# Performance work log

Measured on AMD Instinct MI355X. Metric: run time of the kernel, lower is better.

Reference implementation:

```python
import jax, jax.numpy as jnp
import numpy as np

N_NODES = 50000
N_EDGES = 800000
NFEAT = 256
NHID = 128
LATENT = 64


def setup_inputs() -> dict:
    key = jax.random.key(0)
    ks = jax.random.split(key, 8)
    x = jax.random.normal(ks[0], (N_NODES, NFEAT), dtype=jnp.float32)
    src = jax.random.randint(ks[1], (N_EDGES,), 0, N_NODES, dtype=jnp.int32)
    dst = jax.random.randint(ks[2], (N_EDGES,), 0, N_NODES, dtype=jnp.int32)
    edge_weight = jax.random.uniform(ks[3], (N_EDGES,), dtype=jnp.float32)
    W1 = jax.random.normal(ks[4], (NFEAT, NHID), dtype=jnp.float32) / np.sqrt(NFEAT)
    b1 = jnp.zeros((NHID,), dtype=jnp.float32)
    Wmu = jax.random.normal(ks[5], (NHID, LATENT), dtype=jnp.float32) / np.sqrt(NHID)
    bmu = jnp.zeros((LATENT,), dtype=jnp.float32)
    Wlv = jax.random.normal(ks[6], (NHID, LATENT), dtype=jnp.float32) / np.sqrt(NHID)
    blv = jnp.zeros((LATENT,), dtype=jnp.float32)
    return {"x": x, "src": src, "dst": dst, "edge_weight": edge_weight,
            "W1": W1, "b1": b1, "Wmu": Wmu, "bmu": bmu, "Wlv": Wlv, "blv": blv}


def gcn_conv(x, W, b, src, dst, edge_weight, n_nodes):
    # GCNConv: linear transform then sparse (weighted) adjacency aggregation.
    h = x @ W                                   # [N, out]
    msg = h[src] * edge_weight[:, None]         # [E, out] gather + scale
    agg = jax.ops.segment_sum(msg, dst, num_segments=n_nodes)  # scatter-add
    return agg + b


def reference(x, src, dst, edge_weight, W1, b1, Wmu, bmu, Wlv, blv):
    h = jax.nn.relu(gcn_conv(x, W1, b1, src, dst, edge_weight, N_NODES))
    mu = gcn_conv(h, Wmu, bmu, src, dst, edge_weight, N_NODES)
    logvar = gcn_conv(h, Wlv, blv, src, dst, edge_weight, N_NODES)
    return (mu, logvar)
```

## Files before the change

### kernel.cpp

```cpp
#include <hip/hip_runtime.h>
#include <hip/hip_bf16.h>

#define N_NODES 50000
#define N_EDGES 800000
#define NFEAT 256
#define NHID 128
#define LATENT 64
#define NB 98
#define BSH 9
#define CT 4096
#define CBLK 196

typedef __attribute__((ext_vector_type(8))) short bf16x8;
typedef __attribute__((ext_vector_type(4))) float f32x4;
typedef __attribute__((ext_vector_type(4))) short short4v;
typedef __attribute__((ext_vector_type(8))) short short8v;
typedef __attribute__((ext_vector_type(8))) unsigned short ushort8v;

__device__ inline unsigned short f2bf(float f) {
  union { float f; unsigned u; } c; c.f = f;
  unsigned r = (c.u + 0x7FFFu + ((c.u >> 16) & 1u)) >> 16;
  return (unsigned short)r;
}
__device__ inline float bf2f(unsigned short u) {
  union { unsigned u; float f; } c; c.u = ((unsigned)u) << 16;
  return c.f;
}

__launch_bounds__(256)
__global__ void prep_w_kernel(const float* __restrict__ W1,
                              const float* __restrict__ Wmu,
                              const float* __restrict__ Wlv,
                              unsigned short* __restrict__ W1T,
                              unsigned short* __restrict__ WcT) {
  int b = blockIdx.x;
  int t = threadIdx.x;
  if (b < 128) {
    W1T[b * NFEAT + t] = f2bf(W1[(size_t)t * NHID + b]);
  } else {
    int n = b - 128;
    if (t < NHID) {
      float v = (n < 64) ? Wmu[(size_t)t * LATENT + n]
                         : Wlv[(size_t)t * LATENT + (n - 64)];
      WcT[n * NHID + t] = f2bf(v);
    }
  }
}

__launch_bounds__(256)
__global__ void gemm1_kernel(const float* __restrict__ X,
                             const unsigned short* __restrict__ W1T,
                             unsigned short* __restrict__ XWb) {
  __shared__ short A_lds[64][40];
  const int t = threadIdx.x;
  const int lane = t & 63;
  const int wave = t >> 6;
  const int row0 = blockIdx.x * 64;
  const int l15 = lane & 15, quad = lane >> 4;
  const int srow = t >> 2, skg = t & 3;

  f32x4 acc[4][2];
#pragma unroll
  for (int i = 0; i < 4; i++)
#pragma unroll
    for (int j = 0; j < 2; j++) acc[i][j] = (f32x4){0.f, 0.f, 0.f, 0.f};

  for (int k0 = 0; k0 < NFEAT; k0 += 32) {
    int gr = row0 + srow;
    float4 v0, v1;
    if (gr < N_NODES) {
      const float* p = X + (size_t)gr * NFEAT + k0 + skg * 8;
      v0 = *(const float4*)p;
      v1 = *(const float4*)(p + 4);
    } else {
      v0 = make_float4(0.f, 0.f, 0.f, 0.f);
      v1 = v0;
    }
    short8v s;
    s[0] = f2bf(v0.x); s[1] = f2bf(v0.y); s[2] = f2bf(v0.z); s[3] = f2bf(v0.w);
    s[4] = f2bf(v1.x); s[5] = f2bf(v1.y); s[6] = f2bf(v1.z); s[7] = f2bf(v1.w);
    __syncthreads();
    *(short8v*)&A_lds[srow][skg * 8] = s;
    __syncthreads();

    bf16x8 a[4], b[2];
#pragma unroll
    for (int mt = 0; mt < 4; mt++)
      a[mt] = *(const bf16x8*)&A_lds[mt * 16 + l15][quad * 8];
#pragma unroll
    for (int nt = 0; nt < 2; nt++) {
      int n = wave * 32 + nt * 16 + l15;
      b[nt] = *(const bf16x8*)(W1T + (size_t)n * NFEAT + k0 + quad * 8);
    }
#pragma unroll
    for (int mt = 0; mt < 4; mt++)
#pragma unroll
      for (int nt = 0; nt < 2; nt++)
        acc[mt][nt] = __builtin_amdgcn_mfma_f32_16x16x32_bf16(a[mt], b[nt], acc[mt][nt], 0, 0, 0);
  }
#pragma unroll
  for (int mt = 0; mt < 4; mt++) {
#pragma unroll
    for (int reg = 0; reg < 4; reg++) {
      int gr = row0 + mt * 16 + quad * 4 + reg;
      if (gr < N_NODES) {
#pragma unroll
        for (int nt = 0; nt < 2; nt++) {
          int gc = wave * 32 + nt * 16 + l15;
          XWb[(size_t)gr * NHID + gc] = f2bf(acc[mt][nt][reg]);
        }
      }
    }
  }
}

__launch_bounds__(256)
__global__ void gemm2_kernel(const unsigned short* __restrict__ AGGb,
                             const float* __restrict__ b1,
                             const unsigned short* __restrict__ WcT,
                             unsigned short* __restrict__ Tb) {
  __shared__ short A_lds[64][40];
  const int t = threadIdx.x;
  const int lane = t & 63;
  const int wave = t >> 6;
  const int row0 = blockIdx.x * 64;
  const int l15 = lane & 15, quad = lane >> 4;
  const int srow = t >> 2, skg = t & 3;

  f32x4 acc[4][2];
#pragma unroll
  for (int i = 0; i < 4; i++)
#pragma unroll
    for (int j = 0; j < 2; j++) acc[i][j] = (f32x4){0.f, 0.f, 0.f, 0.f};

  for (int k0 = 0; k0 < NHID; k0 += 32) {
    int gr = row0 + srow;
    const float* bp = b1 + k0 + skg * 8;
    float4 bb0 = *(const float4*)bp;
    float4 bb1 = *(const float4*)(bp + 4);
    float bb[8] = {bb0.x, bb0.y, bb0.z, bb0.w, bb1.x, bb1.y, bb1.z, bb1.w};
    ushort8v raw;
    if (gr < N_NODES) {
      raw = *(const ushort8v*)(AGGb + (size_t)gr * NHID + k0 + skg * 8);
    } else {
#pragma unroll
      for (int k = 0; k < 8; k++) raw[k] = 0;
    }
    short8v s;
#pragma unroll
    for (int k = 0; k < 8; k++)
      s[k] = f2bf(fmaxf(bf2f(raw[k]) + bb[k], 0.f));
    __syncthreads();
    *(short8v*)&A_lds[srow][skg * 8] = s;
    __syncthreads();

    bf16x8 a[4], b[2];
#pragma unroll
    for (int mt = 0; mt < 4; mt++)
      a[mt] = *(const bf16x8*)&A_lds[mt * 16 + l15][quad * 8];
#pragma unroll
    for (int nt = 0; nt < 2; nt++) {
      int n = wave * 32 + nt * 16 + l15;
      b[nt] = *(const bf16x8*)(WcT + (size_t)n * NHID + k0 + quad * 8);
    }
#pragma unroll
    for (int mt = 0; mt < 4; mt++)
#pragma unroll
      for (int nt = 0; nt < 2; nt++)
        acc[mt][nt] = __builtin_amdgcn_mfma_f32_16x16x32_bf16(a[mt], b[nt], acc[mt][nt], 0, 0, 0);
  }
#pragma unroll
  for (int mt = 0; mt < 4; mt++) {
#pragma unroll
    for (int reg = 0; reg < 4; reg++) {
      int gr = row0 + mt * 16 + quad * 4 + reg;
      if (gr < N_NODES) {
#pragma unroll
        for (int nt = 0; nt < 2; nt++) {
          int gc = wave * 32 + nt * 16 + l15;
          Tb[(size_t)gr * NHID + gc] = f2bf(acc[mt][nt][reg]);
        }
      }
    }
  }
}

__launch_bounds__(256)
__global__ void coarse_hist_kernel(const int* __restrict__ dst,
                                   int* __restrict__ chist) {
  __shared__ int h[NB];
  int t = threadIdx.x;
  if (t < NB) h[t] = 0;
  __syncthreads();
  int base = blockIdx.x * CT;
#pragma unroll
  for (int k = 0; k < 16; k++) {
    int e = base + t + k * 256;
    if (e < N_EDGES) atomicAdd(&h[dst[e] >> BSH], 1);
  }
  __syncthreads();
  if (t < NB && h[t]) atomicAdd(&chist[t], h[t]);
}

__launch_bounds__(128)
__global__ void coarse_scan_kernel(const int* __restrict__ chist,
                                   int* __restrict__ coff,
                                   int* __restrict__ bcur) {
  __shared__ int lds[128];
  int t = threadIdx.x;
  int v = (t < NB) ? chist[t] : 0;
  lds[t] = v;
  __syncthreads();
  int x = v;
  for (int ofs = 1; ofs < 128; ofs <<= 1) {
    int y = (t >= ofs) ? lds[t - ofs] : 0;
    __syncthreads();
    x += y;
    lds[t] = x;
    __syncthreads();
  }
  if (t < NB) {
    int o = x - v;
    coff[t] = o;
    bcur[t] = o;
  }
  if (t == NB) coff[NB] = N_EDGES;
}

__launch_bounds__(256)
__global__ void coarse_part_kernel(const int* __restrict__ src,
                                   const int* __restrict__ dst,
                                   const float* __restrict__ ew,
                                   int* __restrict__ bcur,
                                   int2* __restrict__ part) {
  __shared__ int hist[NB], start[NB], cur[NB], gbase[NB];
  __shared__ int sc[128];
  __shared__ int2 stage[CT];
  int t = threadIdx.x;
  if (t < NB) hist[t] = 0;
  __syncthreads();
  int base = blockIdx.x * CT;
#pragma unroll
  for (int k = 0; k < 16; k++) {
    int e = base + t + k * 256;
    if (e < N_EDGES) atomicAdd(&hist[dst[e] >> BSH], 1);
  }
  __syncthreads();
  int v = (t < NB) ? hist[t] : 0;
  if (t < 128) sc[t] = v;
  __syncthreads();
  int x = v;
  for (int ofs = 1; ofs < 128; ofs <<= 1) {
    int y = (t >= ofs && t < 128) ? sc[t - ofs] : 0;
    __syncthreads();
    if (t < 128) { x += y; sc[t] = x; }
    __syncthreads();
  }
  if (t < NB) {
    int st = x - v;
    start[t] = st;
    cur[t] = st;
    gbase[t] = atomicAdd(&bcur[t], hist[t]);
  }
  __syncthreads();
#pragma unroll
  for (int k = 0; k < 16; k++) {
    int e = base + t + k * 256;
    if (e < N_EDGES) {
      int d = dst[e];
      int b = d >> BSH;
      int lp = atomicAdd(&cur[b], 1);
      stage[lp] = make_int2((src[e] << 16) | d, __float_as_int(ew[e]));
    }
  }
  __syncthreads();
  int nedge = min(CT, N_EDGES - base);
  for (int i = t; i < nedge; i += 256) {
    int2 e = stage[i];
    int b = (e.x & 0xffff) >> BSH;
    part[gbase[b] + (i - start[b])] = e;
  }
}

__launch_bounds__(256)
__global__ void fine_kernel(const int* __restrict__ coff,
                            const int2* __restrict__ part,
                            int* __restrict__ off,
                            int2* __restrict__ edata) {
  __shared__ int nh[512];
  __shared__ int sc[256];
  int t = threadIdx.x;
  int b = blockIdx.x;
  int beg = coff[b], end = coff[b + 1];
  int nb = b << BSH;
  nh[t] = 0;
  nh[t + 256] = 0;
  __syncthreads();
  for (int i = beg + t; i < end; i += 256) {
    int d = part[i].x & 0xffff;
    atomicAdd(&nh[d - nb], 1);
  }
  __syncthreads();
  int a0 = nh[2 * t], a1 = nh[2 * t + 1];
  int s = a0 + a1;
  sc[t] = s;
  __syncthreads();
  int x = s;
  for (int ofs = 1; ofs < 256; ofs <<= 1) {
    int y = (t >= ofs) ? sc[t - ofs] : 0;
    __syncthreads();
    x += y;
    sc[t] = x;
    __syncthreads();
  }
  int pairExcl = x - s;
  int e0 = beg + pairExcl;
  int e1 = beg + pairExcl + a0;
  __syncthreads();
  nh[2 * t] = e0;
  nh[2 * t + 1] = e1;
  int g0 = nb + 2 * t, g1 = nb + 2 * t + 1;
  if (g0 <= N_NODES) off[g0] = e0;
  if (g1 <= N_NODES) off[g1] = e1;
  __syncthreads();
  for (int i = beg + t; i < end; i += 256) {
    int2 e = part[i];
    int d = e.x & 0xffff;
    int pos = atomicAdd(&nh[d - nb], 1);
    edata[pos] = make_int2((int)(((unsigned)e.x) >> 16), e.y);
  }
}

__launch_bounds__(256)
__global__ void gather1_kernel(const unsigned short* __restrict__ XWb,
                               const int* __restrict__ off,
                               const int2* __restrict__ edata,
                               unsigned short* __restrict__ aggb) {
  int gw = (int)((blockIdx.x * blockDim.x + threadIdx.x) >> 6);
  if (gw >= N_NODES) return;
  int lane = threadIdx.x & 63;
  int q = lane >> 4;
  int c8 = lane & 15;
  int beg = off[gw], end = off[gw + 1];
  float acc[8];
#pragma unroll
  for (int k = 0; k < 8; k++) acc[k] = 0.f;
  int j = beg + q;
  for (; j + 4 < end; j += 8) {
    int2 e0 = edata[j];
    int2 e1 = edata[j + 4];
    ushort8v r0 = *(const ushort8v*)(XWb + (size_t)e0.x * NHID + c8 * 8);
    ushort8v r1 = *(const ushort8v*)(XWb + (size_t)e1.x * NHID + c8 * 8);
    float w0 = __int_as_float(e0.y);
    float w1 = __int_as_float(e1.y);
#pragma unroll
    for (int k = 0; k < 8; k++) acc[k] += bf2f(r0[k]) * w0;
#pragma unroll
    for (int k = 0; k < 8; k++) acc[k] += bf2f(r1[k]) * w1;
  }
  if (j < end) {
    int2 e0 = edata[j];
    ushort8v r0 = *(const ushort8v*)(XWb + (size_t)e0.x * NHID + c8 * 8);
    float w0 = __int_as_float(e0.y);
#pragma unroll
    for (int k = 0; k < 8; k++) acc[k] += bf2f(r0[k]) * w0;
  }
#pragma unroll
  for (int k = 0; k < 8; k++) {
    acc[k] += __shfl_down(acc[k], 32, 64);
    acc[k] += __shfl_down(acc[k], 16, 64);
  }
  if (lane < 16) {
    ushort8v st;
#pragma unroll
    for (int k = 0; k < 8; k++) st[k] = f2bf(acc[k]);
    *(ushort8v*)(aggb + (size_t)gw * NHID + c8 * 8) = st;
  }
}

__launch_bounds__(256)
__global__ void gather2_kernel(const unsigned short* __restrict__ Tb,
                               const int* __restrict__ off,
                               const int2* __restrict__ edata,
                               const float* __restrict__ bmu,
                               const float* __restrict__ blv,
                               float* __restrict__ out) {
  int gw = (int)((blockIdx.x * blockDim.x + threadIdx.x) >> 6);
  if (gw >= N_NODES) return;
  int lane = threadIdx.x & 63;
  int q = lane >> 4;
  int c8 = lane & 15;
  int beg = off[gw], end = off[gw + 1];
  float acc[8];
#pragma unroll
  for (int k = 0; k < 8; k++) acc[k] = 0.f;
  int j = beg + q;
  for (; j + 4 < end; j += 8) {
    int2 e0 = edata[j];
    int2 e1 = edata[j + 4];
    ushort8v r0 = *(const ushort8v*)(Tb + (size_t)e0.x * NHID + c8 * 8);
    ushort8v r1 = *(const ushort8v*)(Tb + (size_t)e1.x * NHID + c8 * 8);
    float w0 = __int_as_float(e0.y);
    float w1 = __int_as_float(e1.y);
#pragma unroll
    for (int k = 0; k < 8; k++) acc[k] += bf2f(r0[k]) * w0;
#pragma unroll
    for (int k = 0; k < 8; k++) acc[k] += bf2f(r1[k]) * w1;
  }
  if (j < end) {
    int2 e0 = edata[j];
    ushort8v r0 = *(const ushort8v*)(Tb + (size_t)e0.x * NHID + c8 * 8);
    float w0 = __int_as_float(e0.y);
#pragma unroll
    for (int k = 0; k < 8; k++) acc[k] += bf2f(r0[k]) * w0;
  }
#pragma unroll
  for (int k = 0; k < 8; k++) {
    acc[k] += __shfl_down(acc[k], 32, 64);
    acc[k] += __shfl_down(acc[k], 16, 64);
  }
  if (lane < 8) {
    const float* bp = bmu + c8 * 8;
    float4 b0 = *(const float4*)bp;
    float4 b1v = *(const float4*)(bp + 4);
    float* op = out + (size_t)gw * LATENT + c8 * 8;
    float4 o0, o1;
    o0.x = acc[0] + b0.x; o0.y = acc[1] + b0.y;
    o0.z = acc[2] + b0.z; o0.w = acc[3] + b0.w;
    o1.x = acc[4] + b1v.x; o1.y = acc[5] + b1v.y;
    o1.z = acc[6] + b1v.z; o1.w = acc[7] + b1v.w;
    *(float4*)op = o0;
    *(float4*)(op + 4) = o1;
  } else if (lane < 16) {
    int c = c8 - 8;
    const float* bp = blv + c * 8;
    float4 b0 = *(const float4*)bp;
    float4 b1v = *(const float4*)(bp + 4);
    float* op = out + (size_t)N_NODES * LATENT + (size_t)gw * LATENT + c * 8;
    float4 o0, o1;
    o0.x = acc[0] + b0.x; o0.y = acc[1] + b0.y;
    o0.z = acc[2] + b0.z; o0.w = acc[3] + b0.w;
    o1.x = acc[4] + b1v.x; o1.y = acc[5] + b1v.y;
    o1.z = acc[6] + b1v.z; o1.w = acc[7] + b1v.w;
    *(float4*)op = o0;
    *(float4*)(op + 4) = o1;
  }
}

extern "C" void kernel_launch(void* const* d_in, const int* in_sizes, int n_in,
                              void* d_out, int out_size, void* d_ws, size_t ws_size,
                              hipStream_t stream) {
  const float* x   = (const float*)d_in[0];
  const int*   src = (const int*)d_in[1];
  const int*   dst = (const int*)d_in[2];
  const float* ew  = (const float*)d_in[3];
  const float* W1  = (const float*)d_in[4];
  const float* b1  = (const float*)d_in[5];
  const float* Wmu = (const float*)d_in[6];
  const float* bmu = (const float*)d_in[7];
  const float* Wlv = (const float*)d_in[8];
  const float* blv = (const float*)d_in[9];
  float* out = (float*)d_out;

  unsigned short* bufb = (unsigned short*)d_ws;
  unsigned short* aggb = bufb + (size_t)N_NODES * NHID;
  int2* part  = (int2*)(aggb + (size_t)N_NODES * NHID);
  int2* edata = part + N_EDGES;
  int* off    = (int*)(edata + N_EDGES);
  int* chist  = off + 50048;
  int* coff   = chist + 128;
  int* bcur   = coff + 128;
  unsigned short* W1T = (unsigned short*)(bcur + 128);
  unsigned short* WcT = W1T + 128 * NFEAT;

  dim3 blk(256);
  int gemm_grid = (N_NODES + 63) / 64;
  int wave_grid = (N_NODES * 64 + 255) / 256;

  hipMemsetAsync(chist, 0, 128 * sizeof(int), stream);

  prep_w_kernel<<<256, blk, 0, stream>>>(W1, Wmu, Wlv, W1T, WcT);
  gemm1_kernel<<<gemm_grid, blk, 0, stream>>>(x, W1T, bufb);
  coarse_hist_kernel<<<CBLK, blk, 0, stream>>>(dst, chist);
  coarse_scan_kernel<<<1, 128, 0, stream>>>(chist, coff, bcur);
  coarse_part_kernel<<<CBLK, blk, 0, stream>>>(src, dst, ew, bcur, part);
  fine_kernel<<<NB, blk, 0, stream>>>(coff, part, off, edata);

  gather1_kernel<<<wave_grid, blk, 0, stream>>>(bufb, off, edata, aggb);
  gemm2_kernel<<<gemm_grid, blk, 0, stream>>>(aggb, b1, WcT, bufb);
  gather2_kernel<<<wave_grid, blk, 0, stream>>>(bufb, off, edata, bmu, blv, out);
}
```

Baseline: 253.1 us.

## Fuse first aggregation into second GEMM and drop global histogram/scan passes

Removes the coarse histogram and scan kernels by giving each coarse bucket a fixed-capacity slot region (CAP) in the partition buffer, with bucket counters zeroed inside the weight-prep kernel. The fine pass now uses 512 threads and emits (begin,end) pairs plus packed 32-bit edges (16-bit source and bf16 weight). The first gather is fused with the second GEMM so the aggregated hidden tile stays in LDS, which avoids a global round trip and a launch. Risks include bucket overflow if a bucket exceeds CAP, lower weight precision, and lower parallelism in the fused gather, since each wave now handles 16 rows serially.

```diff
diff --git a/kernel.cpp b/kernel.cpp
--- a/kernel.cpp
+++ b/kernel.cpp
@@ -10,10 +10,10 @@
 #define BSH 9
 #define CT 4096
 #define CBLK 196
+#define CAP 8960
 
 typedef __attribute__((ext_vector_type(8))) short bf16x8;
 typedef __attribute__((ext_vector_type(4))) float f32x4;
-typedef __attribute__((ext_vector_type(4))) short short4v;
 typedef __attribute__((ext_vector_type(8))) short short8v;
 typedef __attribute__((ext_vector_type(8))) unsigned short ushort8v;
 
@@ -32,18 +32,21 @@
                               const float* __restrict__ Wmu,
                               const float* __restrict__ Wlv,
                               unsigned short* __restrict__ W1T,
-                              unsigned short* __restrict__ WcT) {
+                              unsigned short* __restrict__ WcT,
+                              int* __restrict__ bcur) {
   int b = blockIdx.x;
   int t = threadIdx.x;
   if (b < 128) {
     W1T[b * NFEAT + t] = f2bf(W1[(size_t)t * NHID + b]);
-  } else {
+  } else if (b < 256) {
     int n = b - 128;
     if (t < NHID) {
       float v = (n < 64) ? Wmu[(size_t)t * LATENT + n]
                          : Wlv[(size_t)t * LATENT + (n - 64)];
       WcT[n * NHID + t] = f2bf(v);
     }
+  } else {
+    if (t < 128) bcur[t] = 0;
   }
 }
 
@@ -114,120 +117,7 @@
   }
 }
 
-__launch_bounds__(256)
-__global__ void gemm2_kernel(const unsigned short* __restrict__ AGGb,
-                             const float* __restrict__ b1,
-                             const unsigned short* __restrict__ WcT,
-                             unsigned short* __restrict__ Tb) {
-  __shared__ short A_lds[64][40];
-  const int t = threadIdx.x;
-  const int lane = t & 63;
-  const int wave = t >> 6;
-  const int row0 = blockIdx.x * 64;
-  const int l15 = lane & 15, quad = lane >> 4;
-  const int srow = t >> 2, skg = t & 3;
-
-  f32x4 acc[4][2];
-#pragma unroll
-  for (int i = 0; i < 4; i++)
-#pragma unroll
-    for (int j = 0; j < 2; j++) acc[i][j] = (f32x4){0.f, 0.f, 0.f, 0.f};
-
-  for (int k0 = 0; k0 < NHID; k0 += 32) {
-    int gr = row0 + srow;
-    const float* bp = b1 + k0 + skg * 8;
-    float4 bb0 = *(const float4*)bp;
-    float4 bb1 = *(const float4*)(bp + 4);
-    float bb[8] = {bb0.x, bb0.y, bb0.z, bb0.w, bb1.x, bb1.y, bb1.z, bb1.w};
-    ushort8v raw;
-    if (gr < N_NODES) {
-      raw = *(const ushort8v*)(AGGb + (size_t)gr * NHID + k0 + skg * 8);
-    } else {
-#pragma unroll
-      for (int k = 0; k < 8; k++) raw[k] = 0;
-    }
-    short8v s;
-#pragma unroll
-    for (int k = 0; k < 8; k++)
-      s[k] = f2bf(fmaxf(bf2f(raw[k]) + bb[k], 0.f));
-    __syncthreads();
-    *(short8v*)&A_lds[srow][skg * 8] = s;
-    __syncthreads();
-
-    bf16x8 a[4], b[2];
-#pragma unroll
-    for (int mt = 0; mt < 4; mt++)
-      a[mt] = *(const bf16x8*)&A_lds[mt * 16 + l15][quad * 8];
-#pragma unroll
-    for (int nt = 0; nt < 2; nt++) {
-      int n = wave * 32 + nt * 16 + l15;
-      b[nt] = *(const bf16x8*)(WcT + (size_t)n * NHID + k0 + quad * 8);
-    }
-#pragma unroll
-    for (int mt = 0; mt < 4; mt++)
-#pragma unroll
-      for (int nt = 0; nt < 2; nt++)
-        acc[mt][nt] = __builtin_amdgcn_mfma_f32_16x16x32_bf16(a[mt], b[nt], acc[mt][nt], 0, 0, 0);
-  }
-#pragma unroll
-  for (int mt = 0; mt < 4; mt++) {
-#pragma unroll
-    for (int reg = 0; reg < 4; reg++) {
-      int gr = row0 + mt * 16 + quad * 4 + reg;
-      if (gr < N_NODES) {
-#pragma unroll
-        for (int nt = 0; nt < 2; nt++) {
-          int gc = wave * 32 + nt * 16 + l15;
-          Tb[(size_t)gr * NHID + gc] = f2bf(acc[mt][nt][reg]);
-        }
-      }
-    }
-  }
-}
-
-__launch_bounds__(256)
-__global__ void coarse_hist_kernel(const int* __restrict__ dst,
-                                   int* __restrict__ chist) {
-  __shared__ int h[NB];
-  int t = threadIdx.x;
-  if (t < NB) h[t] = 0;
-  __syncthreads();
-  int base = blockIdx.x * CT;
-#pragma unroll
-  for (int k = 0; k < 16; k++) {
-    int e = base + t + k * 256;
-    if (e < N_EDGES) atomicAdd(&h[dst[e] >> BSH], 1);
-  }
-  __syncthreads();
-  if (t < NB && h[t]) atomicAdd(&chist[t], h[t]);
-}
-
-__launch_bounds__(128)
-__global__ void coarse_scan_kernel(const int* __restrict__ chist,
-                                   int* __restrict__ coff,
-                                   int* __restrict__ bcur) {
-  __shared__ int lds[128];
-  int t = threadIdx.x;
-  int v = (t < NB) ? chist[t] : 0;
-  lds[t] = v;
-  __syncthreads();
-  int x = v;
-  for (int ofs = 1; ofs < 128; ofs <<= 1) {
-    int y = (t >= ofs) ? lds[t - ofs] : 0;
-    __syncthreads();
-    x += y;
-    lds[t] = x;
-    __syncthreads();
-  }
-  if (t < NB) {
-    int o = x - v;
-    coff[t] = o;
-    bcur[t] = o;
-  }
-  if (t == NB) coff[NB] = N_EDGES;
-}
-
-__launch_bounds__(256)
+__launch_bounds__(512)
 __global__ void coarse_part_kernel(const int* __restrict__ src,
                                    const int* __restrict__ dst,
                                    const float* __restrict__ ew,
@@ -241,8 +131,8 @@
   __syncthreads();
   int base = blockIdx.x * CT;
 #pragma unroll
-  for (int k = 0; k < 16; k++) {
-    int e = base + t + k * 256;
+  for (int k = 0; k < 8; k++) {
+    int e = base + t + k * 512;
     if (e < N_EDGES) atomicAdd(&hist[dst[e] >> BSH], 1);
   }
   __syncthreads();
@@ -264,8 +154,8 @@
   }
   __syncthreads();
 #pragma unroll
-  for (int k = 0; k < 16; k++) {
-    int e = base + t + k * 256;
+  for (int k = 0; k < 8; k++) {
+    int e = base + t + k * 512;
     if (e < N_EDGES) {
       int d = dst[e];
       int b = d >> BSH;
@@ -275,113 +165,160 @@
   }
   __syncthreads();
   int nedge = min(CT, N_EDGES - base);
-  for (int i = t; i < nedge; i += 256) {
+  for (int i = t; i < nedge; i += 512) {
     int2 e = stage[i];
     int b = (e.x & 0xffff) >> BSH;
-    part[gbase[b] + (i - start[b])] = e;
-  }
-}
-
-__launch_bounds__(256)
-__global__ void fine_kernel(const int* __restrict__ coff,
+    part[(size_t)b * CAP + gbase[b] + (i - start[b])] = e;
+  }
+}
+
+__launch_bounds__(512)
+__global__ void fine_kernel(const int* __restrict__ bcur,
                             const int2* __restrict__ part,
-                            int* __restrict__ off,
-                            int2* __restrict__ edata) {
+                            int2* __restrict__ offs,
+                            unsigned int* __restrict__ edata) {
   __shared__ int nh[512];
-  __shared__ int sc[256];
+  __shared__ int sc[512];
   int t = threadIdx.x;
   int b = blockIdx.x;
-  int beg = coff[b], end = coff[b + 1];
+  int base = b * CAP;
+  int cnt = bcur[b];
   int nb = b << BSH;
   nh[t] = 0;
-  nh[t + 256] = 0;
-  __syncthreads();
-  for (int i = beg + t; i < end; i += 256) {
-    int d = part[i].x & 0xffff;
+  __syncthreads();
+  for (int i = t; i < cnt; i += 512) {
+    int d = part[base + i].x & 0xffff;
     atomicAdd(&nh[d - nb], 1);
   }
   __syncthreads();
-  int a0 = nh[2 * t], a1 = nh[2 * t + 1];
-  int s = a0 + a1;
-  sc[t] = s;
-  __syncthreads();
-  int x = s;
-  for (int ofs = 1; ofs < 256; ofs <<= 1) {
+  int v = nh[t];
+  sc[t] = v;
+  __syncthreads();
+  int x = v;
+  for (int ofs = 1; ofs < 512; ofs <<= 1) {
     int y = (t >= ofs) ? sc[t - ofs] : 0;
     __syncthreads();
     x += y;
     sc[t] = x;
     __syncthreads();
   }
-  int pairExcl = x - s;
-  int e0 = beg + pairExcl;
-  int e1 = beg + pairExcl + a0;
-  __syncthreads();
-  nh[2 * t] = e0;
-  nh[2 * t + 1] = e1;
-  int g0 = nb + 2 * t, g1 = nb + 2 * t + 1;
-  if (g0 <= N_NODES) off[g0] = e0;
-  if (g1 <= N_NODES) off[g1] = e1;
-  __syncthreads();
-  for (int i = beg + t; i < end; i += 256) {
-    int2 e = part[i];
+  int beg = base + (x - v);
+  offs[nb + t] = make_int2(beg, beg + v);
+  nh[t] = beg;
+  __syncthreads();
+  for (int i = t; i < cnt; i += 512) {
+    int2 e = part[base + i];
     int d = e.x & 0xffff;
     int pos = atomicAdd(&nh[d - nb], 1);
-    edata[pos] = make_int2((int)(((unsigned)e.x) >> 16), e.y);
+    edata[pos] = (unsigned)(e.x & 0xffff0000) | (unsigned)f2bf(__int_as_float(e.y));
   }
 }
 
 __launch_bounds__(256)
-__global__ void gather1_kernel(const unsigned short* __restrict__ XWb,
-                               const int* __restrict__ off,
-                               const int2* __restrict__ edata,
-                               unsigned short* __restrict__ aggb) {
-  int gw = (int)((blockIdx.x * blockDim.x + threadIdx.x) >> 6);
-  if (gw >= N_NODES) return;
-  int lane = threadIdx.x & 63;
-  int q = lane >> 4;
-  int c8 = lane & 15;
-  int beg = off[gw], end = off[gw + 1];
-  float acc[8];
-#pragma unroll
-  for (int k = 0; k < 8; k++) acc[k] = 0.f;
-  int j = beg + q;
-  for (; j + 4 < end; j += 8) {
-    int2 e0 = edata[j];
-    int2 e1 = edata[j + 4];
-    ushort8v r0 = *(const ushort8v*)(XWb + (size_t)e0.x * NHID + c8 * 8);
-    ushort8v r1 = *(const ushort8v*)(XWb + (size_t)e1.x * NHID + c8 * 8);
-    float w0 = __int_as_float(e0.y);
-    float w1 = __int_as_float(e1.y);
-#pragma unroll
-    for (int k = 0; k < 8; k++) acc[k] += bf2f(r0[k]) * w0;
-#pragma unroll
-    for (int k = 0; k < 8; k++) acc[k] += bf2f(r1[k]) * w1;
-  }
-  if (j < end) {
-    int2 e0 = edata[j];
-    ushort8v r0 = *(const ushort8v*)(XWb + (size_t)e0.x * NHID + c8 * 8);
-    float w0 = __int_as_float(e0.y);
-#pragma unroll
-    for (int k = 0; k < 8; k++) acc[k] += bf2f(r0[k]) * w0;
-  }
-#pragma unroll
-  for (int k = 0; k < 8; k++) {
-    acc[k] += __shfl_down(acc[k], 32, 64);
-    acc[k] += __shfl_down(acc[k], 16, 64);
-  }
-  if (lane < 16) {
-    ushort8v st;
-#pragma unroll
-    for (int k = 0; k < 8; k++) st[k] = f2bf(acc[k]);
-    *(ushort8v*)(aggb + (size_t)gw * NHID + c8 * 8) = st;
+__global__ void g1gemm2_kernel(const unsigned short* __restrict__ XWb,
+                               const int2* __restrict__ offs,
+                               const unsigned int* __restrict__ edata,
+                               const float* __restrict__ b1,
+                               const unsigned short* __restrict__ WcT,
+                               unsigned short* __restrict__ Tb) {
+  __shared__ short A_lds[64][136];
+  const int t = threadIdx.x;
+  const int lane = t & 63;
+  const int wave = t >> 6;
+  const int row0 = blockIdx.x * 64;
+  const int l15 = lane & 15, quad = lane >> 4;
+
+  float bb[8];
+#pragma unroll
+  for (int k = 0; k < 8; k++) bb[k] = b1[l15 * 8 + k];
+
+  for (int r = 0; r < 16; r++) {
+    int row = wave * 16 + r;
+    int gw = row0 + row;
+    float acc[8];
+#pragma unroll
+    for (int k = 0; k < 8; k++) acc[k] = 0.f;
+    if (gw < N_NODES) {
+      int2 oo = offs[gw];
+      int j = oo.x + quad;
+      int end = oo.y;
+      for (; j + 4 < end; j += 8) {
+        unsigned e0 = edata[j];
+        unsigned e1 = edata[j + 4];
+        ushort8v r0 = *(const ushort8v*)(XWb + (size_t)(e0 >> 16) * NHID + l15 * 8);
+        ushort8v r1 = *(const ushort8v*)(XWb + (size_t)(e1 >> 16) * NHID + l15 * 8);
+        float w0 = bf2f((unsigned short)(e0 & 0xffffu));
+        float w1 = bf2f((unsigned short)(e1 & 0xffffu));
+#pragma unroll
+        for (int k = 0; k < 8; k++) acc[k] += bf2f(r0[k]) * w0;
+#pragma unroll
+        for (int k = 0; k < 8; k++) acc[k] += bf2f(r1[k]) * w1;
+      }
+      if (j < end) {
+        unsigned e0 = edata[j];
+        ushort8v r0 = *(const ushort8v*)(XWb + (size_t)(e0 >> 16) * NHID + l15 * 8);
+        float w0 = bf2f((unsigned short)(e0 & 0xffffu));
+#pragma unroll
+        for (int k = 0; k < 8; k++) acc[k] += bf2f(r0[k]) * w0;
+      }
+    }
+#pragma unroll
+    for (int k = 0; k < 8; k++) {
+      acc[k] += __shfl_down(acc[k], 32, 64);
+      acc[k] += __shfl_down(acc[k], 16, 64);
+    }
+    if (lane < 16) {
+      short8v s;
+#pragma unroll
+      for (int k = 0; k < 8; k++) s[k] = (short)f2bf(fmaxf(acc[k] + bb[k], 0.f));
+      *(short8v*)&A_lds[row][l15 * 8] = s;
+    }
+  }
+  __syncthreads();
+
+  f32x4 acc2[4][2];
+#pragma unroll
+  for (int i = 0; i < 4; i++)
+#pragma unroll
+    for (int j = 0; j < 2; j++) acc2[i][j] = (f32x4){0.f, 0.f, 0.f, 0.f};
+
+#pragma unroll
+  for (int k0 = 0; k0 < NHID; k0 += 32) {
+    bf16x8 a[4], b[2];
+#pragma unroll
+    for (int mt = 0; mt < 4; mt++)
+      a[mt] = *(const bf16x8*)&A_lds[mt * 16 + l15][k0 + quad * 8];
+#pragma unroll
+    for (int nt = 0; nt < 2; nt++) {
+      int n = wave * 32 + nt * 16 + l15;
+      b[nt] = *(const bf16x8*)(WcT + (size_t)n * NHID + k0 + quad * 8);
+    }
+#pragma unroll
+    for (int mt = 0; mt < 4; mt++)
+#pragma unroll
+      for (int nt = 0; nt < 2; nt++)
+        acc2[mt][nt] = __builtin_amdgcn_mfma_f32_16x16x32_bf16(a[mt], b[nt], acc2[mt][nt], 0, 0, 0);
+  }
+#pragma unroll
+  for (int mt = 0; mt < 4; mt++) {
+#pragma unroll
+    for (int reg = 0; reg < 4; reg++) {
+      int gr = row0 + mt * 16 + quad * 4 + reg;
+      if (gr < N_NODES) {
+#pragma unroll
+        for (int nt = 0; nt < 2; nt++) {
+          int gc = wave * 32 + nt * 16 + l15;
+          Tb[(size_t)gr * NHID + gc] = f2bf(acc2[mt][nt][reg]);
+        }
+      }
+    }
   }
 }
 
 __launch_bounds__(256)
 __global__ void gather2_kernel(const unsigned short* __restrict__ Tb,
-                               const int* __restrict__ off,
-                               const int2* __restrict__ edata,
+                               const int2* __restrict__ offs,
+                               const unsigned int* __restrict__ edata,
                                const float* __restrict__ bmu,
                                const float* __restrict__ blv,
                                float* __restrict__ out) {
@@ -390,27 +327,28 @@
   int lane = threadIdx.x & 63;
   int q = lane >> 4;
   int c8 = lane & 15;
-  int beg = off[gw], end = off[gw + 1];
+  int2 oo = offs[gw];
+  int end = oo.y;
   float acc[8];
 #pragma unroll
   for (int k = 0; k < 8; k++) acc[k] = 0.f;
-  int j = beg + q;
+  int j = oo.x + q;
   for (; j + 4 < end; j += 8) {
-    int2 e0 = edata[j];
-    int2 e1 = edata[j + 4];
-    ushort8v r0 = *(const ushort8v*)(Tb + (size_t)e0.x * NHID + c8 * 8);
-    ushort8v r1 = *(const ushort8v*)(Tb + (size_t)e1.x * NHID + c8 * 8);
-    float w0 = __int_as_float(e0.y);
-    float w1 = __int_as_float(e1.y);
+    unsigned e0 = edata[j];
+    unsigned e1 = edata[j + 4];
+    ushort8v r0 = *(const ushort8v*)(Tb + (size_t)(e0 >> 16) * NHID + c8 * 8);
+    ushort8v r1 = *(const ushort8v*)(Tb + (size_t)(e1 >> 16) * NHID + c8 * 8);
+    float w0 = bf2f((unsigned short)(e0 & 0xffffu));
+    float w1 = bf2f((unsigned short)(e1 & 0xffffu));
 #pragma unroll
     for (int k = 0; k < 8; k++) acc[k] += bf2f(r0[k]) * w0;
 #pragma unroll
     for (int k = 0; k < 8; k++) acc[k] += bf2f(r1[k]) * w1;
   }
   if (j < end) {
-    int2 e0 = edata[j];
-    ushort8v r0 = *(const ushort8v*)(Tb + (size_t)e0.x * NHID + c8 * 8);
-    float w0 = __int_as_float(e0.y);
+    unsigned e0 = edata[j];
+    ushort8v r0 = *(const ushort8v*)(Tb + (size_t)(e0 >> 16) * NHID + c8 * 8);
+    float w0 = bf2f((unsigned short)(e0 & 0xffffu));
 #pragma unroll
     for (int k = 0; k < 8; k++) acc[k] += bf2f(r0[k]) * w0;
   }
@@ -462,14 +400,12 @@
   const float* blv = (const float*)d_in[9];
   float* out = (float*)d_out;
 
-  unsigned short* bufb = (unsigned short*)d_ws;
-  unsigned short* aggb = bufb + (size_t)N_NODES * NHID;
-  int2* part  = (int2*)(aggb + (size_t)N_NODES * NHID);
-  int2* edata = part + N_EDGES;
-  int* off    = (int*)(edata + N_EDGES);
-  int* chist  = off + 50048;
-  int* coff   = chist + 128;
-  int* bcur   = coff + 128;
+  unsigned short* XWb = (unsigned short*)d_ws;
+  unsigned short* Tbb = XWb + (size_t)N_NODES * NHID;
+  int2* part = (int2*)(Tbb + (size_t)N_NODES * NHID);
+  unsigned int* edata = (unsigned int*)(part + (size_t)NB * CAP);
+  int2* offs = (int2*)(edata + (size_t)NB * CAP);
+  int* bcur  = (int*)(offs + 50176);
   unsigned short* W1T = (unsigned short*)(bcur + 128);
   unsigned short* WcT = W1T + 128 * NFEAT;
 
@@ -477,16 +413,10 @@
   int gemm_grid = (N_NODES + 63) / 64;
   int wave_grid = (N_NODES * 64 + 255) / 256;
 
-  hipMemsetAsync(chist, 0, 128 * sizeof(int), stream);
-
-  prep_w_kernel<<<256, blk, 0, stream>>>(W1, Wmu, Wlv, W1T, WcT);
-  gemm1_kernel<<<gemm_grid, blk, 0, stream>>>(x, W1T, bufb);
-  coarse_hist_kernel<<<CBLK, blk, 0, stream>>>(dst, chist);
-  coarse_scan_kernel<<<1, 128, 0, stream>>>(chist, coff, bcur);
-  coarse_part_kernel<<<CBLK, blk, 0, stream>>>(src, dst, ew, bcur, part);
-  fine_kernel<<<NB, blk, 0, stream>>>(coff, part, off, edata);
-
-  gather1_kernel<<<wave_grid, blk, 0, stream>>>(bufb, off, edata, aggb);
-  gemm2_kernel<<<gemm_grid, blk, 0, stream>>>(aggb, b1, WcT, bufb);
-  gather2_kernel<<<wave_grid, blk, 0, stream>>>(bufb, off, edata, bmu, blv, out);
-}
+  prep_w_kernel<<<257, blk, 0, stream>>>(W1, Wmu, Wlv, W1T, WcT, bcur);
+  gemm1_kernel<<<gemm_grid, blk, 0, stream>>>(x, W1T, XWb);
+  coarse_part_kernel<<<CBLK, dim3(512), 0, stream>>>(src, dst, ew, bcur, part);
+  fine_kernel<<<NB, dim3(512), 0, stream>>>(bcur, part, offs, edata);
+  g1gemm2_kernel<<<gemm_grid, blk, 0, stream>>>(XWb, offs, edata, b1, WcT, Tbb);
+  gather2_kernel<<<wave_grid, blk, 0, stream>>>(Tbb, offs, edata, bmu, blv, out);
+}
```

Result: faster. 230.3 us (-9.0%).
